# Kernel tuning notes

Measured on AMD Instinct MI355X. Metric: run time of the kernel, lower is better.

The kernel has to match this reference:

```python
import jax, jax.numpy as jnp
import numpy as np

B, C, H, W = 16, 64, 128, 128
K = 3  # dynamic kernel size


def setup_inputs() -> dict:
    key = jax.random.key(0)
    ks = jax.random.split(key, 6)
    return {
        "x": jax.random.normal(ks[0], (B, C, H, W), jnp.float32),       # feature map
        "d": jax.random.normal(ks[1], (B, 64), jnp.float32),            # degradation repr
        "Wk1": jax.random.normal(ks[2], (64, 64), jnp.float32) * 0.05,  # Linear(64,64), no bias
        "Wk2": jax.random.normal(ks[3], (64 * K * K, 64), jnp.float32) * 0.05,  # Linear(64,576)
        "Wc": jax.random.normal(ks[4], (64, 64), jnp.float32) * 0.05,   # 1x1 conv weight (out,in)
        "bc": jnp.zeros((64,), jnp.float32),                            # 1x1 conv bias
    }


def _lrelu(v):
    return jnp.where(v >= 0, v, 0.1 * v)


def reference(x, d, Wk1, Wk2, Wc, bc):
    b, c, h, w = x.shape
    k = K
    # kernel-generating MLP: Linear -> LeakyReLU(0.1) -> Linear
    hid = _lrelu(d @ Wk1.T)                      # (B, 64)
    kern = (hid @ Wk2.T).reshape(b, c, 1, k, k)   # one 3x3 kernel per (batch, channel)

    # dynamic depthwise 3x3 conv: per-sample kernels, groups == channels
    def dwconv(xi, ki):
        # xi: (C,H,W), ki: (C,1,3,3) in OIHW with feature_group_count=C
        return jax.lax.conv_general_dilated(
            xi[None], ki, window_strides=(1, 1), padding='SAME',
            feature_group_count=c,
            dimension_numbers=('NCHW', 'OIHW', 'NCHW'))[0]

    out = jax.vmap(dwconv)(x, kern)              # (B,C,H,W)
    out = _lrelu(out)
    # 1x1 pointwise conv with bias
    out = jnp.einsum('bchw,oc->bohw', out, Wc) + bc[None, :, None, None]
    return out
```

## Files before the change

kernel.cpp:

```cpp
#include <hip/hip_runtime.h>

#define Bn 16
#define Cn 64
#define Hn 128
#define Wn 128
#define HWn (Hn * Wn)

typedef __attribute__((ext_vector_type(8)))  short  short8;
typedef __attribute__((ext_vector_type(16))) float  floatx16;
typedef __attribute__((ext_vector_type(4)))  float  floatx4;
using int32x4 = int __attribute__((ext_vector_type(4)));

__device__ float
llvm_amdgcn_raw_buffer_load_fp32(int32x4 srsrc, int voffset, int soffset,
                                 int aux) __asm("llvm.amdgcn.raw.buffer.load.f32");
__device__ floatx4
llvm_amdgcn_raw_buffer_load_v4f32(int32x4 srsrc, int voffset, int soffset,
                                  int aux) __asm("llvm.amdgcn.raw.buffer.load.v4f32");

__device__ __forceinline__ int32x4 make_rsrc(const void* p, int bytes) {
    int32x4 r;
    r.x = (int)(unsigned)(uintptr_t)p;
    r.y = (int)((uintptr_t)p >> 32);
    r.z = bytes;
    r.w = 0x00020000;
    return r;
}

__device__ __forceinline__ unsigned short f2bf(float f) {
    unsigned u = __float_as_uint(f);
    u += 0x7fffu + ((u >> 16) & 1u);
    return (unsigned short)(u >> 16);
}
__device__ __forceinline__ float lrelu(float v) { return v >= 0.f ? v : 0.1f * v; }

__global__ __launch_bounds__(192)
void gen_kern6(const float* __restrict__ d,
               const float* __restrict__ Wk1,
               const float* __restrict__ Wk2,
               const float* __restrict__ Wc,
               float* __restrict__ kernP,
               unsigned short* __restrict__ WcBF) {
    const int b = blockIdx.x;
    const int r = blockIdx.y;
    const int t = threadIdx.x;
    __shared__ float hid_s[64];

    if (t < 64) {
        const float4* __restrict__ w4 = (const float4*)(Wk1 + (size_t)t * 64);
        const float*  __restrict__ db = d + b * 64;
        float s0 = 0.f, s1 = 0.f, s2 = 0.f, s3 = 0.f;
        #pragma unroll
        for (int j = 0; j < 16; ++j) {
            const float4 wv = w4[j];
            s0 += db[4 * j + 0] * wv.x;
            s1 += db[4 * j + 1] * wv.y;
            s2 += db[4 * j + 2] * wv.z;
            s3 += db[4 * j + 3] * wv.w;
        }
        hid_s[t] = lrelu((s0 + s1) + (s2 + s3));
    }
    __syncthreads();

    {
        const int o = r * 192 + t;
        const float4* __restrict__ w4 = (const float4*)(Wk2 + (size_t)o * 64);
        const float4* __restrict__ h4 = (const float4*)hid_s;
        float s0 = 0.f, s1 = 0.f, s2 = 0.f, s3 = 0.f;
        #pragma unroll
        for (int j = 0; j < 16; ++j) {
            const float4 wv = w4[j];
            const float4 hv = h4[j];
            s0 += hv.x * wv.x;
            s1 += hv.y * wv.y;
            s2 += hv.z * wv.z;
            s3 += hv.w * wv.w;
        }
        const int c = o / 9, tap = o - c * 9;
        kernP[b * 768 + c * 12 + tap] = (s0 + s1) + (s2 + s3);
    }

    if (b == 0 && r == 0) {
        for (int idx = t; idx < 4096; idx += 192)
            WcBF[idx] = f2bf(Wc[idx]);
    }
}

struct XK { floatx4 x[3][2]; };

__device__ __forceinline__ void issue_x(XK& v, int32x4 rs, int c,
                                        const int* rofsB, int px0) {
    #pragma unroll
    for (int r = 0; r < 3; ++r) {
        const int vo = (c << 16) + rofsB[r] + px0 * 4;
        v.x[r][0] = llvm_amdgcn_raw_buffer_load_v4f32(rs, vo, 0, 0);
        v.x[r][1] = llvm_amdgcn_raw_buffer_load_v4f32(rs, vo + 16, 0, 0);
    }
}

__device__ __forceinline__ short8 compute_dw(const XK& v, const float* kp,
                                             int c, int lane, int tm) {
    const floatx4* k4 = (const floatx4*)(kp + c * 12);
    const floatx4 k0 = k4[0];
    const floatx4 k1 = k4[1];
    const float   k8 = ((const float*)k4)[8];

    float t0[8], t1[8], t2[8];
    #pragma unroll
    for (int i = 0; i < 8; ++i) {
        const float xr0 = (i < 4) ? v.x[0][0][i] : v.x[0][1][i - 4];
        const float xr1 = (i < 4) ? v.x[1][0][i] : v.x[1][1][i - 4];
        const float xr2 = (i < 4) ? v.x[2][0][i] : v.x[2][1][i - 4];
        t0[i] = k0.x * xr0 + k0.w * xr1 + k1.z * xr2;
        t1[i] = k0.y * xr0 + k1.x * xr1 + k1.w * xr2;
        t2[i] = k0.z * xr0 + k1.y * xr1 + k8   * xr2;
    }
    float t0m = __shfl(t0[7], lane - 1, 64);
    float t2p = __shfl(t2[0], lane + 1, 64);
    if (tm == 0)  t0m = 0.f;
    if (tm == 15) t2p = 0.f;

    float dw[8];
    dw[0] = t0m + t1[0] + t2[1];
    #pragma unroll
    for (int i = 1; i < 7; ++i) dw[i] = t0[i - 1] + t1[i] + t2[i + 1];
    dw[7] = t0[6] + t1[7] + t2p;

    short8 w8;
    #pragma unroll
    for (int i = 0; i < 8; ++i) w8[i] = (short)f2bf(lrelu(dw[i]));
    return w8;
}

__global__ __launch_bounds__(256)
void da_mfma3(const float* __restrict__ x,
              const float* __restrict__ kernP,
              const unsigned short* __restrict__ WcBF,
              const float* __restrict__ bc,
              float* __restrict__ out) {
    const int t    = threadIdx.x;
    const int lane = t & 63;
    const int wv   = t >> 6;
    const int col  = lane & 31;
    const int kh   = lane >> 5;
    const int bx   = blockIdx.x;
    const int h    = ((bx & 7) << 4) | (bx >> 3);
    const int b    = blockIdx.y;
    const int px   = wv * 32 + col;

    const int sch = t >> 4;
    const int tm  = t & 15;
    const int px0 = tm * 8;

    __shared__ unsigned short dwB[2][2048];

    int rofsB[3];
    #pragma unroll
    for (int i = 0; i < 3; ++i) {
        const int hh = h + i - 1;
        rofsB[i] = (hh >= 0 && hh < Hn) ? hh * (Wn * 4) : 0x10000000;
    }

    const int32x4 rs = make_rsrc(x + (size_t)b * Cn * HWn, Cn * HWn * 4);
    const float* __restrict__ kp = kernP + b * 768;

    floatx16 acc[2];
    #pragma unroll
    for (int m = 0; m < 2; ++m)
        #pragma unroll
        for (int r = 0; r < 16; ++r)
            acc[m][r] = bc[m * 32 + (r & 3) + 8 * (r >> 2) + 4 * kh];

    {
        XK cur;
        issue_x(cur, rs, sch, rofsB, px0);
        const short8 w8 = compute_dw(cur, kp, sch, lane, tm);
        *(short8*)&dwB[0][sch * 128 + (px0 ^ ((sch & 8) << 2))] = w8;
    }
    __syncthreads();

    #pragma unroll
    for (int g = 0; g < 4; ++g) {
        XK nxt;
        if (g < 3)
            issue_x(nxt, rs, (g + 1) * 16 + sch, rofsB, px0);

        short8 bfr;
        #pragma unroll
        for (int j = 0; j < 8; ++j) {
            const int cl = kh * 8 + j;
            bfr[j] = (short)dwB[g & 1][cl * 128 + (px ^ ((cl & 8) << 2))];
        }
        const short8 a0 = *(const short8*)(WcBF + (0 * 32 + col) * 64 + g * 16 + kh * 8);
        const short8 a1 = *(const short8*)(WcBF + (1 * 32 + col) * 64 + g * 16 + kh * 8);
        acc[0] = __builtin_amdgcn_mfma_f32_32x32x16_bf16(a0, bfr, acc[0], 0, 0, 0);
        acc[1] = __builtin_amdgcn_mfma_f32_32x32x16_bf16(a1, bfr, acc[1], 0, 0, 0);

        if (g < 3) {
            const short8 w8 = compute_dw(nxt, kp, (g + 1) * 16 + sch, lane, tm);
            *(short8*)&dwB[(g + 1) & 1][sch * 128 + (px0 ^ ((sch & 8) << 2))] = w8;
            __syncthreads();
        }
    }

    float* __restrict__ ob = out + (size_t)b * Cn * HWn + h * Wn + px;
    #pragma unroll
    for (int m = 0; m < 2; ++m)
        #pragma unroll
        for (int r = 0; r < 16; ++r) {
            const int o = m * 32 + (r & 3) + 8 * (r >> 2) + 4 * kh;
            ob[(size_t)o * HWn] = acc[m][r];
        }
}

extern "C" void kernel_launch(void* const* d_in, const int* in_sizes, int n_in,
                              void* d_out, int out_size, void* d_ws, size_t ws_size,
                              hipStream_t stream) {
    const float* x   = (const float*)d_in[0];
    const float* d   = (const float*)d_in[1];
    const float* Wk1 = (const float*)d_in[2];
    const float* Wk2 = (const float*)d_in[3];
    const float* Wc  = (const float*)d_in[4];
    const float* bc  = (const float*)d_in[5];
    float* out = (float*)d_out;
    float*          kernP = (float*)d_ws;
    unsigned short* WcBF  = (unsigned short*)((float*)d_ws + Bn * 768);

    gen_kern6<<<dim3(Bn, 3), dim3(192), 0, stream>>>(d, Wk1, Wk2, Wc, kernP, WcBF);
    da_mfma3<<<dim3(Hn, Bn), dim3(256), 0, stream>>>(x, kernP, WcBF, bc, out);
}
```

Measured before the change: 137.1 us.

## Deepen load prefetch to two stages and use lightweight LDS barriers

The fused depthwise+pointwise kernel now issues the x row loads two channel-groups ahead instead of one. It also prefetches the per-channel dynamic kernel taps and the bf16 Wc fragments one step ahead. The bias add moves from the accumulator init to the epilogue as vectorized float4 loads, and __syncthreads is replaced by an inline s_waitcnt lgkmcnt(0)+s_barrier that does not wait on outstanding global loads. This aims to hide global-memory latency behind the MFMA and dwconv work, at the cost of higher register pressure (four XK buffers) and possibly lower occupancy.

```diff
diff --git a/kernel.cpp b/kernel.cpp
--- a/kernel.cpp
+++ b/kernel.cpp
@@ -11,9 +11,6 @@
 typedef __attribute__((ext_vector_type(4)))  float  floatx4;
 using int32x4 = int __attribute__((ext_vector_type(4)));
 
-__device__ float
-llvm_amdgcn_raw_buffer_load_fp32(int32x4 srsrc, int voffset, int soffset,
-                                 int aux) __asm("llvm.amdgcn.raw.buffer.load.f32");
 __device__ floatx4
 llvm_amdgcn_raw_buffer_load_v4f32(int32x4 srsrc, int voffset, int soffset,
                                   int aux) __asm("llvm.amdgcn.raw.buffer.load.v4f32");
@@ -33,6 +30,8 @@
     return (unsigned short)(u >> 16);
 }
 __device__ __forceinline__ float lrelu(float v) { return v >= 0.f ? v : 0.1f * v; }
+
+#define SYNC_LDS() asm volatile("s_waitcnt lgkmcnt(0)\n\ts_barrier" ::: "memory")
 
 __global__ __launch_bounds__(192)
 void gen_kern6(const float* __restrict__ d,
@@ -87,6 +86,7 @@
 }
 
 struct XK { floatx4 x[3][2]; };
+struct KF { floatx4 k0, k1; float k8; };
 
 __device__ __forceinline__ void issue_x(XK& v, int32x4 rs, int c,
                                         const int* rofsB, int px0) {
@@ -98,22 +98,24 @@
     }
 }
 
-__device__ __forceinline__ short8 compute_dw(const XK& v, const float* kp,
-                                             int c, int lane, int tm) {
+__device__ __forceinline__ void issue_k(KF& kf, const float* kp, int c) {
     const floatx4* k4 = (const floatx4*)(kp + c * 12);
-    const floatx4 k0 = k4[0];
-    const floatx4 k1 = k4[1];
-    const float   k8 = ((const float*)k4)[8];
-
+    kf.k0 = k4[0];
+    kf.k1 = k4[1];
+    kf.k8 = ((const float*)k4)[8];
+}
+
+__device__ __forceinline__ short8 compute_dw(const XK& v, const KF& kf,
+                                             int lane, int tm) {
     float t0[8], t1[8], t2[8];
     #pragma unroll
     for (int i = 0; i < 8; ++i) {
         const float xr0 = (i < 4) ? v.x[0][0][i] : v.x[0][1][i - 4];
         const float xr1 = (i < 4) ? v.x[1][0][i] : v.x[1][1][i - 4];
         const float xr2 = (i < 4) ? v.x[2][0][i] : v.x[2][1][i - 4];
-        t0[i] = k0.x * xr0 + k0.w * xr1 + k1.z * xr2;
-        t1[i] = k0.y * xr0 + k1.x * xr1 + k1.w * xr2;
-        t2[i] = k0.z * xr0 + k1.y * xr1 + k8   * xr2;
+        t0[i] = kf.k0.x * xr0 + kf.k0.w * xr1 + kf.k1.z * xr2;
+        t1[i] = kf.k0.y * xr0 + kf.k1.x * xr1 + kf.k1.w * xr2;
+        t2[i] = kf.k0.z * xr0 + kf.k1.y * xr1 + kf.k8   * xr2;
     }
     float t0m = __shfl(t0[7], lane - 1, 64);
     float t2p = __shfl(t2[0], lane + 1, 64);
@@ -133,7 +135,7 @@
 }
 
 __global__ __launch_bounds__(256)
-void da_mfma3(const float* __restrict__ x,
+void da_mfma4(const float* __restrict__ x,
               const float* __restrict__ kernP,
               const unsigned short* __restrict__ WcBF,
               const float* __restrict__ bc,
@@ -169,21 +171,29 @@
     for (int m = 0; m < 2; ++m)
         #pragma unroll
         for (int r = 0; r < 16; ++r)
-            acc[m][r] = bc[m * 32 + (r & 3) + 8 * (r >> 2) + 4 * kh];
-
+            acc[m][r] = 0.f;
+
+    XK X[4]; KF Kf[4]; short8 a0[4], a1[4];
+    a0[0] = *(const short8*)(WcBF + (0 * 32 + col) * 64 + 0 * 16 + kh * 8);
+    a1[0] = *(const short8*)(WcBF + (1 * 32 + col) * 64 + 0 * 16 + kh * 8);
+    issue_k(Kf[0], kp, sch);
+    issue_k(Kf[1], kp, 16 + sch);
+    issue_x(X[0], rs, sch, rofsB, px0);
+    issue_x(X[1], rs, 16 + sch, rofsB, px0);
     {
-        XK cur;
-        issue_x(cur, rs, sch, rofsB, px0);
-        const short8 w8 = compute_dw(cur, kp, sch, lane, tm);
+        const short8 w8 = compute_dw(X[0], Kf[0], lane, tm);
         *(short8*)&dwB[0][sch * 128 + (px0 ^ ((sch & 8) << 2))] = w8;
     }
-    __syncthreads();
+    SYNC_LDS();
 
     #pragma unroll
     for (int g = 0; g < 4; ++g) {
-        XK nxt;
-        if (g < 3)
-            issue_x(nxt, rs, (g + 1) * 16 + sch, rofsB, px0);
+        if (g < 2) issue_x(X[g + 2], rs, (g + 2) * 16 + sch, rofsB, px0);
+        if (g < 3) {
+            a0[g + 1] = *(const short8*)(WcBF + (0 * 32 + col) * 64 + (g + 1) * 16 + kh * 8);
+            a1[g + 1] = *(const short8*)(WcBF + (1 * 32 + col) * 64 + (g + 1) * 16 + kh * 8);
+        }
+        if (g < 2) issue_k(Kf[g + 2], kp, (g + 2) * 16 + sch);
 
         short8 bfr;
         #pragma unroll
@@ -191,15 +201,13 @@
             const int cl = kh * 8 + j;
             bfr[j] = (short)dwB[g & 1][cl * 128 + (px ^ ((cl & 8) << 2))];
         }
-        const short8 a0 = *(const short8*)(WcBF + (0 * 32 + col) * 64 + g * 16 + kh * 8);
-        const short8 a1 = *(const short8*)(WcBF + (1 * 32 + col) * 64 + g * 16 + kh * 8);
-        acc[0] = __builtin_amdgcn_mfma_f32_32x32x16_bf16(a0, bfr, acc[0], 0, 0, 0);
-        acc[1] = __builtin_amdgcn_mfma_f32_32x32x16_bf16(a1, bfr, acc[1], 0, 0, 0);
+        acc[0] = __builtin_amdgcn_mfma_f32_32x32x16_bf16(a0[g], bfr, acc[0], 0, 0, 0);
+        acc[1] = __builtin_amdgcn_mfma_f32_32x32x16_bf16(a1[g], bfr, acc[1], 0, 0, 0);
 
         if (g < 3) {
-            const short8 w8 = compute_dw(nxt, kp, (g + 1) * 16 + sch, lane, tm);
+            const short8 w8 = compute_dw(X[g + 1], Kf[g + 1], lane, tm);
             *(short8*)&dwB[(g + 1) & 1][sch * 128 + (px0 ^ ((sch & 8) << 2))] = w8;
-            __syncthreads();
+            SYNC_LDS();
         }
     }
 
@@ -207,9 +215,13 @@
     #pragma unroll
     for (int m = 0; m < 2; ++m)
         #pragma unroll
-        for (int r = 0; r < 16; ++r) {
-            const int o = m * 32 + (r & 3) + 8 * (r >> 2) + 4 * kh;
-            ob[(size_t)o * HWn] = acc[m][r];
+        for (int q = 0; q < 4; ++q) {
+            const float4 bv = *(const float4*)&bc[m * 32 + q * 8 + 4 * kh];
+            #pragma unroll
+            for (int j = 0; j < 4; ++j) {
+                const int o = m * 32 + q * 8 + 4 * kh + j;
+                ob[(size_t)o * HWn] = acc[m][q * 4 + j] + ((const float*)&bv)[j];
+            }
         }
 }
 
@@ -227,5 +239,5 @@
     unsigned short* WcBF  = (unsigned short*)((float*)d_ws + Bn * 768);
 
     gen_kern6<<<dim3(Bn, 3), dim3(192), 0, stream>>>(d, Wk1, Wk2, Wc, kernP, WcBF);
-    da_mfma3<<<dim3(Hn, Bn), dim3(256), 0, stream>>>(x, kernP, WcBF, bc, out);
-}
+    da_mfma4<<<dim3(Hn, Bn), dim3(256), 0, stream>>>(x, kernP, WcBF, bc, out);
+}
```

Measured after the change: 138.5 us. No clear change (+1.0%).
